# Optimization experiments

Measured on AMD Instinct MI355X. Metric: run time of the kernel, lower is better.

## Reference

```python
import jax, jax.numpy as jnp
import numpy as np


def setup_inputs() -> dict:
    key = jax.random.key(0)
    x = jax.random.normal(key, (32, 1024, 1024), dtype=jnp.float32)
    return {"x": x}


def reference(x) -> jnp.ndarray:
    # Orthonormal DCT-II along axis 1 via length-2n FFT of [x, reverse(x)],
    # matching tf dct_odd_case numerics (complex64 path, real part taken).
    N, n, m = x.shape
    nf = jnp.float32(n)
    # y = [x; flip(x, axis=1)] -> length 2n along axis 1
    y = jnp.concatenate([x, x[:, ::-1, :]], axis=1)
    F = jnp.fft.fft(y.astype(jnp.complex64), axis=1)[:, :n, :]  # [N, n, m] complex64
    k = jnp.arange(n, dtype=jnp.float32)
    # twiddle: exp(-i*pi*k/(2n)) / sqrt(2n), with k=0 term divided by sqrt(2)
    phase = -k * (jnp.pi / (2.0 * nf))
    t = (jnp.cos(phase) + 1j * jnp.sin(phase)).astype(jnp.complex64) / jnp.sqrt(2.0 * nf)
    scale0 = jnp.where(k == 0, 1.0 / jnp.sqrt(jnp.float32(2.0)), jnp.float32(1.0))
    t = t * scale0.astype(jnp.complex64)
    dct_x = jnp.real(t[None, :, None] * F)  # [N, n, m] float32
    return dct_x
```

## Files before the change

### kernel.cpp

```cpp
#include <hip/hip_runtime.h>
#include <hip/hip_bf16.h>
#include <math.h>

typedef __bf16 bf16_8 __attribute__((ext_vector_type(8)));
typedef float f32x4 __attribute__((ext_vector_type(4)));

#define NDIM 1024

__device__ static inline void async_copy16(const void* g, void* l) {
  __builtin_amdgcn_global_load_lds(
      (__attribute__((address_space(1))) void*)g,
      (__attribute__((address_space(3))) void*)l, 16, 0, 0);
}


__global__ void gen_dct_blocked(__bf16* __restrict__ A) {
  int idx = blockIdx.x * blockDim.x + threadIdx.x;
  int m = idx >> 7;
  int ks = idx & 127;
  int kt = ks >> 3, s = ks & 7;
  int mt = m >> 7, r = m & 127;
  float sc = (m == 0) ? 0.03125f : 0.04419417382415922f;
  int kbase = kt * 64 + s * 8;
  bf16_8 v;
#pragma unroll
  for (int q = 0; q < 8; q++) {
    int k = kbase + q;
    int t = (m * (2 * k + 1)) & 4095;
    float ang = (float)t * 1.5339807878856412e-3f;
    v[q] = (__bf16)(sc * cosf(ang));
  }
  *(bf16_8*)(A + (((size_t)(mt * 16 + kt)) << 13) + r * 64 + ((s ^ (r & 7)) << 3)) = v;
}

#define TP 132
__global__ __launch_bounds__(256) void transpose_cvt(const float* __restrict__ x,
                                                     __bf16* __restrict__ B) {
  __shared__ float T[64 * TP];
  const int t = threadIdx.x;
  const int kt = blockIdx.x, nt = blockIdx.y, b = blockIdx.z;
  const float* xb =
      x + (size_t)b * (NDIM * NDIM) + (size_t)kt * 64 * NDIM + nt * 128;
  {
    const int kr = t >> 5;
    const int c4 = (t & 31) * 4;
#pragma unroll
    for (int u = 0; u < 8; u++) {
      int k = u * 8 + kr;
      f32x4 v = *(const f32x4*)(xb + (size_t)k * NDIM + c4);
      *(f32x4*)(&T[k * TP + c4]) = v;
    }
  }
  __syncthreads();
  __bf16* img = B + (((size_t)((b * 8 + nt) * 16 + kt)) << 13);
#pragma unroll
  for (int u = 0; u < 4; u++) {
    int c = t * 4 + u;
    int r = c >> 3, sp = c & 7;
    int s = sp ^ (r & 7);
    bf16_8 v;
#pragma unroll
    for (int q = 0; q < 8; q++) v[q] = (__bf16)T[(s * 8 + q) * TP + r];
    *(bf16_8*)(img + c * 8) = v;
  }
}

__global__ __launch_bounds__(256) void dct_gemm2(const __bf16* __restrict__ A,
                                                 const __bf16* __restrict__ B,
                                                 float* __restrict__ out) {
  __shared__ __align__(1024) __bf16 As[2][128 * 64];
  __shared__ __align__(1024) __bf16 Bs[2][128 * 64];
  const int t = threadIdx.x;
  const int w = t >> 6, lane = t & 63;
  const int nt = blockIdx.x, mt = blockIdx.y, b = blockIdx.z;

  const __bf16* ag = A + (((size_t)mt * 16) << 13) + w * 2048 + lane * 8;
  const __bf16* bg =
      B + (((size_t)((b * 8 + nt) * 16)) << 13) + w * 2048 + lane * 8;

  const int r16 = lane & 15;
  const int g8 = (lane >> 4) << 3;
  const int wm = (w & 1) << 6, wn = (w >> 1) << 6;
  const int xr = (r16 & 7) << 3;
  const int kof0 = g8 ^ xr;
  const int kof1 = (32 + g8) ^ xr;

#pragma unroll
  for (int i = 0; i < 4; i++) {
    async_copy16(ag + i * 512, &As[0][w * 2048 + i * 512]);
    async_copy16(bg + i * 512, &Bs[0][w * 2048 + i * 512]);
  }
  __syncthreads();

  f32x4 acc[4][4] = {};

  for (int kt = 0; kt < 16; kt++) {
    const int cur = kt & 1;
    if (kt < 15) {
      const __bf16* an = ag + (size_t)(kt + 1) * 8192;
      const __bf16* bn = bg + (size_t)(kt + 1) * 8192;
      const int nb = cur ^ 1;
#pragma unroll
      for (int i = 0; i < 4; i++) {
        async_copy16(an + i * 512, &As[nb][w * 2048 + i * 512]);
        async_copy16(bn + i * 512, &Bs[nb][w * 2048 + i * 512]);
      }
    }
    const __bf16* as = &As[cur][0];
    const __bf16* bs = &Bs[cur][0];
#pragma unroll
    for (int h = 0; h < 2; h++) {
      const int kof = h ? kof1 : kof0;
      bf16_8 af[4], bfr[4];
#pragma unroll
      for (int i = 0; i < 4; i++)
        af[i] = *(const bf16_8*)(as + (wm + i * 16 + r16) * 64 + kof);
#pragma unroll
      for (int j = 0; j < 4; j++)
        bfr[j] = *(const bf16_8*)(bs + (wn + j * 16 + r16) * 64 + kof);
#pragma unroll
      for (int i = 0; i < 4; i++)
#pragma unroll
        for (int j = 0; j < 4; j++)
          acc[i][j] = __builtin_amdgcn_mfma_f32_16x16x32_bf16(af[i], bfr[j],
                                                              acc[i][j], 0, 0, 0);
    }
    __syncthreads();
  }

  float* ob = out + (size_t)b * (NDIM * NDIM);
  const int rbase = (lane >> 4) << 2;
  const int cofs = lane & 15;
  const int m0 = mt * 128, n0 = nt * 128;
#pragma unroll
  for (int i = 0; i < 4; i++)
#pragma unroll
    for (int rr = 0; rr < 4; rr++) {
      int row = m0 + wm + i * 16 + rbase + rr;
#pragma unroll
      for (int j = 0; j < 4; j++) {
        int col = n0 + wn + j * 16 + cofs;
        ob[(size_t)row * NDIM + col] = acc[i][j][rr];
      }
    }
}

#define BM 128
#define BN 128
#define BK 32
#define BSTRIDE 40

__global__ void gen_dct_mat(__bf16* __restrict__ C) {
  int idx = blockIdx.x * blockDim.x + threadIdx.x;
  int k = idx >> 10;
  int j = idx & 1023;
  int t = (k * (2 * j + 1)) & 4095;
  float ang = (float)t * 1.5339807878856412e-3f;
  float s = (k == 0) ? 0.03125f : 0.04419417382415922f;
  C[idx] = (__bf16)(s * cosf(ang));
}

__global__ __launch_bounds__(256) void dct_gemm(
    const float* __restrict__ x, const __bf16* __restrict__ A,
    float* __restrict__ out) {
  __shared__ __align__(64) __bf16 Asm[BM * BK];
  __shared__ __align__(64) __bf16 Bsm[BN * BSTRIDE];

  const int t = threadIdx.x;
  const int wave = t >> 6;
  const int lane = t & 63;
  const int bb = blockIdx.z;
  const int m0 = blockIdx.y * BM;
  const int n0 = blockIdx.x * BN;

  const __bf16* Ag0 =
      A + (size_t)(m0 + wave * 16 + (lane >> 2)) * NDIM + ((lane & 3) * 8);
  const __bf16* Ag1 = Ag0 + (size_t)64 * NDIM;
  __bf16* Al0 = Asm + (wave * 16) * BK;
  __bf16* Al1 = Asm + (64 + wave * 16) * BK;

  const int bc = t & 127;
  const int bjg = t >> 7;
  const float* xs =
      x + (size_t)bb * (NDIM * NDIM) + (size_t)(bjg * 16) * NDIM + (n0 + bc);
  bf16_8* bs0 = (bf16_8*)(Bsm + bc * BSTRIDE + bjg * 16);
  bf16_8* bs1 = (bf16_8*)(Bsm + bc * BSTRIDE + bjg * 16 + 8);

  const int row16 = lane & 15;
  const int kq8 = (lane >> 4) * 8;
  const int wm = (wave & 1) * 64;
  const int wn = (wave >> 1) * 64;

  f32x4 acc[4][4] = {};

  for (int k0 = 0; k0 < NDIM; k0 += BK) {
    __syncthreads();
    async_copy16(Ag0 + k0, Al0);
    async_copy16(Ag1 + k0, Al1);

    const float* xp = xs + (size_t)k0 * NDIM;
    bf16_8 v0, v1;
#pragma unroll
    for (int q = 0; q < 8; q++) {
      v0[q] = (__bf16)xp[(size_t)q * NDIM];
      v1[q] = (__bf16)xp[(size_t)(q + 8) * NDIM];
    }
    *bs0 = v0;
    *bs1 = v1;
    __syncthreads();

    bf16_8 af[4], bfr[4];
#pragma unroll
    for (int i = 0; i < 4; i++)
      af[i] = *(const bf16_8*)(Asm + (wm + i * 16 + row16) * BK + kq8);
#pragma unroll
    for (int j = 0; j < 4; j++)
      bfr[j] = *(const bf16_8*)(Bsm + (wn + j * 16 + row16) * BSTRIDE + kq8);
#pragma unroll
    for (int i = 0; i < 4; i++)
#pragma unroll
      for (int j = 0; j < 4; j++)
        acc[i][j] = __builtin_amdgcn_mfma_f32_16x16x32_bf16(af[i], bfr[j],
                                                            acc[i][j], 0, 0, 0);
  }

  float* ob = out + (size_t)bb * (NDIM * NDIM);
  const int rbase = (lane >> 4) * 4;
  const int cofs = lane & 15;
#pragma unroll
  for (int i = 0; i < 4; i++) {
#pragma unroll
    for (int r = 0; r < 4; r++) {
      int row = m0 + wm + i * 16 + rbase + r;
#pragma unroll
      for (int j = 0; j < 4; j++) {
        int col = n0 + wn + j * 16 + cofs;
        ob[(size_t)row * NDIM + col] = acc[i][j][r];
      }
    }
  }
}

extern "C" void kernel_launch(void* const* d_in, const int* in_sizes, int n_in,
                              void* d_out, int out_size, void* d_ws,
                              size_t ws_size, hipStream_t stream) {
  const float* x = (const float*)d_in[0];
  float* out = (float*)d_out;

  const size_t need = (size_t)66 * 1024 * 1024;
  if (ws_size >= need) {
    __bf16* Ab = (__bf16*)d_ws;
    __bf16* Bb = Ab + (size_t)1024 * 1024;
    gen_dct_blocked<<<dim3(512), dim3(256), 0, stream>>>(Ab);
    transpose_cvt<<<dim3(16, 8, 32), dim3(256), 0, stream>>>(x, Bb);
    dct_gemm2<<<dim3(8, 8, 32), dim3(256), 0, stream>>>(Ab, Bb, out);
  } else {
    __bf16* Cmat = (__bf16*)d_ws;
    gen_dct_mat<<<dim3((NDIM * NDIM) / 256), dim3(256), 0, stream>>>(Cmat);
    dct_gemm<<<dim3(NDIM / BN, NDIM / BM, 32), dim3(256), 0, stream>>>(x, Cmat,
                                                                       out);
  }
}
```

Before: 302.2 us.

## Exploit DCT-II even/odd symmetry to halve GEMM reduction length

```diff
diff --git a/kernel.cpp b/kernel.cpp
--- a/kernel.cpp
+++ b/kernel.cpp
@@ -3,6 +3,7 @@
 #include <math.h>
 
 typedef __bf16 bf16_8 __attribute__((ext_vector_type(8)));
+typedef __bf16 bf16_4 __attribute__((ext_vector_type(4)));
 typedef float f32x4 __attribute__((ext_vector_type(4)));
 
 #define NDIM 1024
@@ -14,69 +15,88 @@
 }
 
 
-__global__ void gen_dct_blocked(__bf16* __restrict__ A) {
+__global__ void gen_dct_fold(__bf16* __restrict__ A) {
   int idx = blockIdx.x * blockDim.x + threadIdx.x;
-  int m = idx >> 7;
-  int ks = idx & 127;
-  int kt = ks >> 3, s = ks & 7;
-  int mt = m >> 7, r = m & 127;
-  float sc = (m == 0) ? 0.03125f : 0.04419417382415922f;
-  int kbase = kt * 64 + s * 8;
+  int sel = idx >> 15;
+  int rem = idx & 32767;
+  int mp = rem >> 6;
+  int slot = rem & 63;
+  int kt = slot >> 3, s = slot & 7;
+  int k = 2 * mp + sel;
+  int r = mp & 127, mtp = mp >> 7;
+  float sc = (k == 0) ? 0.03125f : 0.04419417382415922f;
+  int jb = kt * 64 + s * 8;
   bf16_8 v;
 #pragma unroll
   for (int q = 0; q < 8; q++) {
-    int k = kbase + q;
-    int t = (m * (2 * k + 1)) & 4095;
+    int j = jb + q;
+    int t = (k * (2 * j + 1)) & 4095;
     float ang = (float)t * 1.5339807878856412e-3f;
     v[q] = (__bf16)(sc * cosf(ang));
   }
-  *(bf16_8*)(A + (((size_t)(mt * 16 + kt)) << 13) + r * 64 + ((s ^ (r & 7)) << 3)) = v;
-}
-
-#define TP 132
-__global__ __launch_bounds__(256) void transpose_cvt(const float* __restrict__ x,
-                                                     __bf16* __restrict__ B) {
-  __shared__ float T[64 * TP];
+  *(bf16_8*)(A + (((size_t)(sel * 32 + mtp * 8 + kt)) << 13) + r * 64 +
+             ((s ^ (r & 7)) << 3)) = v;
+}
+
+__global__ __launch_bounds__(256) void fold_cvt(const float* __restrict__ x,
+                                                __bf16* __restrict__ B) {
+  __shared__ __bf16 Tu[64 * 128];
+  __shared__ __bf16 Tv[64 * 128];
   const int t = threadIdx.x;
   const int kt = blockIdx.x, nt = blockIdx.y, b = blockIdx.z;
-  const float* xb =
-      x + (size_t)b * (NDIM * NDIM) + (size_t)kt * 64 * NDIM + nt * 128;
-  {
-    const int kr = t >> 5;
-    const int c4 = (t & 31) * 4;
-#pragma unroll
-    for (int u = 0; u < 8; u++) {
-      int k = u * 8 + kr;
-      f32x4 v = *(const f32x4*)(xb + (size_t)k * NDIM + c4);
-      *(f32x4*)(&T[k * TP + c4]) = v;
-    }
+  const float* xb = x + (size_t)b * (NDIM * NDIM) + nt * 128;
+  const int kr = t >> 5;
+  const int c4 = (t & 31) * 4;
+  const int jb = kt * 64;
+  const int mb = 1023 - kt * 64;
+#pragma unroll
+  for (int u = 0; u < 8; u++) {
+    int k = u * 8 + kr;
+    f32x4 a = *(const f32x4*)(xb + (size_t)(jb + k) * NDIM + c4);
+    f32x4 m = *(const f32x4*)(xb + (size_t)(mb - k) * NDIM + c4);
+    f32x4 su = a + m, dv = a - m;
+    bf16_4 wu, wv;
+#pragma unroll
+    for (int i = 0; i < 4; i++) {
+      wu[i] = (__bf16)su[i];
+      wv[i] = (__bf16)dv[i];
+    }
+    *(bf16_4*)(&Tu[k * 128 + c4]) = wu;
+    *(bf16_4*)(&Tv[k * 128 + c4]) = wv;
   }
   __syncthreads();
-  __bf16* img = B + (((size_t)((b * 8 + nt) * 16 + kt)) << 13);
+  __bf16* outU = B + (((size_t)(b * 2 + 0) * 64 + nt * 8 + kt) << 13);
+  __bf16* outV = B + (((size_t)(b * 2 + 1) * 64 + nt * 8 + kt) << 13);
 #pragma unroll
   for (int u = 0; u < 4; u++) {
     int c = t * 4 + u;
     int r = c >> 3, sp = c & 7;
     int s = sp ^ (r & 7);
-    bf16_8 v;
-#pragma unroll
-    for (int q = 0; q < 8; q++) v[q] = (__bf16)T[(s * 8 + q) * TP + r];
-    *(bf16_8*)(img + c * 8) = v;
-  }
-}
-
-__global__ __launch_bounds__(256) void dct_gemm2(const __bf16* __restrict__ A,
+    bf16_8 vU, vV;
+#pragma unroll
+    for (int q = 0; q < 8; q++) {
+      vU[q] = Tu[(s * 8 + q) * 128 + r];
+      vV[q] = Tv[(s * 8 + q) * 128 + r];
+    }
+    *(bf16_8*)(outU + c * 8) = vU;
+    *(bf16_8*)(outV + c * 8) = vV;
+  }
+}
+
+__global__ __launch_bounds__(256) void dct_gemm3(const __bf16* __restrict__ A,
                                                  const __bf16* __restrict__ B,
                                                  float* __restrict__ out) {
   __shared__ __align__(1024) __bf16 As[2][128 * 64];
   __shared__ __align__(1024) __bf16 Bs[2][128 * 64];
   const int t = threadIdx.x;
   const int w = t >> 6, lane = t & 63;
-  const int nt = blockIdx.x, mt = blockIdx.y, b = blockIdx.z;
-
-  const __bf16* ag = A + (((size_t)mt * 16) << 13) + w * 2048 + lane * 8;
+  const int nt = blockIdx.x, b = blockIdx.z;
+  const int sel = blockIdx.y & 1, mtp = blockIdx.y >> 1;
+
+  const __bf16* ag =
+      A + (((size_t)(sel * 32 + mtp * 8)) << 13) + w * 2048 + lane * 8;
   const __bf16* bg =
-      B + (((size_t)((b * 8 + nt) * 16)) << 13) + w * 2048 + lane * 8;
+      B + (((size_t)(b * 2 + sel) * 64 + nt * 8) << 13) + w * 2048 + lane * 8;
 
   const int r16 = lane & 15;
   const int g8 = (lane >> 4) << 3;
@@ -94,9 +114,9 @@
 
   f32x4 acc[4][4] = {};
 
-  for (int kt = 0; kt < 16; kt++) {
+  for (int kt = 0; kt < 8; kt++) {
     const int cur = kt & 1;
-    if (kt < 15) {
+    if (kt < 7) {
       const __bf16* an = ag + (size_t)(kt + 1) * 8192;
       const __bf16* bn = bg + (size_t)(kt + 1) * 8192;
       const int nb = cur ^ 1;
@@ -131,12 +151,13 @@
   float* ob = out + (size_t)b * (NDIM * NDIM);
   const int rbase = (lane >> 4) << 2;
   const int cofs = lane & 15;
-  const int m0 = mt * 128, n0 = nt * 128;
+  const int n0 = nt * 128;
 #pragma unroll
   for (int i = 0; i < 4; i++)
 #pragma unroll
     for (int rr = 0; rr < 4; rr++) {
-      int row = m0 + wm + i * 16 + rbase + rr;
+      int rh = mtp * 128 + wm + i * 16 + rbase + rr;
+      int row = rh * 2 + sel;
 #pragma unroll
       for (int j = 0; j < 4; j++) {
         int col = n0 + wn + j * 16 + cofs;
@@ -250,10 +271,10 @@
   const size_t need = (size_t)66 * 1024 * 1024;
   if (ws_size >= need) {
     __bf16* Ab = (__bf16*)d_ws;
-    __bf16* Bb = Ab + (size_t)1024 * 1024;
-    gen_dct_blocked<<<dim3(512), dim3(256), 0, stream>>>(Ab);
-    transpose_cvt<<<dim3(16, 8, 32), dim3(256), 0, stream>>>(x, Bb);
-    dct_gemm2<<<dim3(8, 8, 32), dim3(256), 0, stream>>>(Ab, Bb, out);
+    __bf16* Bb = (__bf16*)((char*)d_ws + (size_t)2 * 1024 * 1024);
+    gen_dct_fold<<<dim3(256), dim3(256), 0, stream>>>(Ab);
+    fold_cvt<<<dim3(8, 8, 32), dim3(256), 0, stream>>>(x, Bb);
+    dct_gemm3<<<dim3(8, 8, 32), dim3(256), 0, stream>>>(Ab, Bb, out);
   } else {
     __bf16* Cmat = (__bf16*)d_ws;
     gen_dct_mat<<<dim3((NDIM * NDIM) / 256), dim3(256), 0, stream>>>(Cmat);
```

Measured after the change: 279.7 us. 1.08x faster.
